# Performance work log

Hardware: AMD Instinct MI355X
Metric: run time of the kernel (lower is better)

The kernel has to match this reference:

```python
import jax, jax.numpy as jnp
import numpy as np

B, D, H, W = 1, 16, 16, 16
C, NH = 528, 8
HD = C // NH      # 66
K = 32            # retrieved memories per token


def setup_inputs() -> dict:
    key = jax.random.key(0)
    ks = jax.random.split(key, 4)
    x = jax.random.normal(ks[0], (B, D, H, W, C), jnp.float32)
    # simulated knn_memory.search output: (B, heads, N, K, 2[k/v], head_dim)
    knn_kv = jax.random.normal(ks[1], (B, NH, D * H * W, K, 2, HD), jnp.float32)
    w_qkv = jax.random.normal(ks[2], (3 * C, C), jnp.float32) * 0.02
    b_qkv = jnp.zeros((3 * C,), jnp.float32)
    w_proj = jax.random.normal(ks[3], (C, C), jnp.float32) * 0.02
    b_proj = jnp.zeros((C,), jnp.float32)
    return {"x": x, "knn_kv": knn_kv, "w_qkv": w_qkv, "b_qkv": b_qkv,
            "w_proj": w_proj, "b_proj": b_proj, "num_heads": NH}


def _l2norm(t):
    # F.normalize(t, dim=-1): t / max(||t||_2, eps)
    n = jnp.linalg.norm(t, axis=-1, keepdims=True)
    return t / jnp.maximum(n, 1e-12)


def _forward(x, knn_kv, w_qkv, b_qkv, w_proj, b_proj, num_heads):
    Bb, Dd, Hh, Ww, Cc = x.shape
    N = Dd * Hh * Ww
    hd = Cc // num_heads
    scaling = hd ** -0.5
    qkv = x.reshape(Bb * N, Cc) @ w_qkv.T + b_qkv
    qkv = qkv.reshape(Bb, N, 3, num_heads, hd).transpose(2, 0, 3, 1, 4)  # (3,B,h,N,hd)
    q, k, v = qkv[0], qkv[1], qkv[2]
    q = _l2norm(q)
    k = _l2norm(k)
    knn_k = knn_kv[..., 0, :]   # (B,h,N,K,hd)
    knn_v = knn_kv[..., 1, :]
    k_comb = jnp.concatenate([knn_k, k[..., None, :]], axis=-2)  # (B,h,N,K+1,hd)
    v_comb = jnp.concatenate([knn_v, v[..., None, :]], axis=-2)
    attn = jnp.einsum('bhnd,bhnkd->bhnk', q, k_comb) * scaling
    attn = jax.nn.softmax(attn, axis=-1)  # stable softmax
    out = jnp.einsum('bhnk,bhnkd->bhnd', attn, v_comb)  # (B,h,N,hd)
    out = out.transpose(0, 2, 1, 3).reshape(Bb * N, num_heads * hd)
    out = out @ w_proj.T + b_proj
    return out.reshape(Bb, Dd, Hh, Ww, Cc)


def reference(x, knn_kv, w_qkv, b_qkv, w_proj, b_proj, num_heads):
    return _forward(x, knn_kv, w_qkv, b_qkv, w_proj, b_proj, num_heads)
```

## Files before the change

### kernel.cpp

```cpp
#include <hip/hip_runtime.h>
#include <hip/hip_bf16.h>
#include <math.h>

#define N_POS 4096
#define C_DIM 528
#define NHEAD 8
#define HDIM  66
#define KNN   32
#define CQKV  1584
#define KP    544
#define NP1   1664
#define NP2   640

typedef __attribute__((ext_vector_type(8))) short short8;
typedef __attribute__((ext_vector_type(4))) float f32x4;
typedef __hip_bfloat16 bf16;

__global__ __launch_bounds__(256) void convpad3_kernel(
    const float* __restrict__ x, const float* __restrict__ wq,
    const float* __restrict__ wp,
    bf16* __restrict__ xb, bf16* __restrict__ wqb, bf16* __restrict__ wpb)
{
    int b = blockIdx.x;
    const float* src; bf16* dst; int Nr;
    if (b < N_POS)            { src = x;  dst = xb;  Nr = N_POS; }
    else if (b < N_POS + NP1) { b -= N_POS; src = wq; dst = wqb; Nr = CQKV; }
    else                      { b -= N_POS + NP1; src = wp; dst = wpb; Nr = C_DIM; }
    for (int c = threadIdx.x; c < KP; c += 256) {
        float v = (b < Nr && c < C_DIM) ? src[(size_t)b * C_DIM + c] : 0.0f;
        dst[(size_t)b * KP + c] = __float2bfloat16(v);
    }
}

template <bool BF16OUT>
__global__ __launch_bounds__(256) void gemm_mfma_kernel(
    const bf16* __restrict__ A, const bf16* __restrict__ B,
    const float* __restrict__ bias, void* __restrict__ Cv,
    int Nreal, int ldc, int nbx)
{
    __shared__ short8 As[512];
    __shared__ short8 Bs[512];

    const int tid  = threadIdx.x;
    const int lane = tid & 63;
    const int wid  = tid >> 6;

    const int nwg   = gridDim.x;
    const int chunk = nwg >> 3;
    const int swz   = (blockIdx.x & 7) * chunk + (blockIdx.x >> 3);
    const int bm = (swz / nbx) * 128;
    const int bn = (swz % nbx) * 128;

    const int r0 = tid >> 2;
    const int c0 = tid & 3;
    const bf16* Ag = A + (size_t)(bm + r0) * KP + c0 * 8;
    const bf16* Bg = B + (size_t)(bn + r0) * KP + c0 * 8;
    const size_t roff = (size_t)64 * KP;

    short8 a0 = *(const short8*)(Ag);
    short8 a1 = *(const short8*)(Ag + roff);
    short8 b0 = *(const short8*)(Bg);
    short8 b1 = *(const short8*)(Bg + roff);

    const int w0 = r0 * 4 + (c0 ^ (r0 & 3));
    const int w1 = w0 + 256;

    const int wm = (wid >> 1) * 64;
    const int wn = (wid & 1) * 64;
    const int arow = wm + (lane & 15);
    const int brow = wn + (lane & 15);
    const int apc  = lane >> 4;
    const int aslot = arow * 4 + (apc ^ (arow & 3));
    const int bslot = brow * 4 + (apc ^ (brow & 3));

    f32x4 acc[4][4];
    #pragma unroll
    for (int i = 0; i < 4; ++i)
        #pragma unroll
        for (int j = 0; j < 4; ++j)
            acc[i][j] = (f32x4){0.f, 0.f, 0.f, 0.f};

    for (int k0 = 0;; k0 += 32) {
        As[w0] = a0; As[w1] = a1;
        Bs[w0] = b0; Bs[w1] = b1;
        __syncthreads();
        if (k0 + 32 < KP) {
            const bf16* An = Ag + (k0 + 32);
            const bf16* Bn = Bg + (k0 + 32);
            a0 = *(const short8*)(An);
            a1 = *(const short8*)(An + roff);
            b0 = *(const short8*)(Bn);
            b1 = *(const short8*)(Bn + roff);
        }
        short8 af[4], bfr[4];
        #pragma unroll
        for (int f = 0; f < 4; ++f) af[f]  = As[aslot + f * 64];
        #pragma unroll
        for (int f = 0; f < 4; ++f) bfr[f] = Bs[bslot + f * 64];
        #pragma unroll
        for (int i = 0; i < 4; ++i)
            #pragma unroll
            for (int j = 0; j < 4; ++j)
                acc[i][j] = __builtin_amdgcn_mfma_f32_16x16x32_bf16(
                    af[i], bfr[j], acc[i][j], 0, 0, 0);
        if (k0 + 32 >= KP) break;
        __syncthreads();
    }

    #pragma unroll
    for (int i = 0; i < 4; ++i) {
        const int row = bm + wm + i * 16 + (lane >> 4) * 4;
        #pragma unroll
        for (int j = 0; j < 4; ++j) {
            const int col = bn + wn + j * 16 + (lane & 15);
            if (col < Nreal) {
                const float bv = bias[col];
                #pragma unroll
                for (int r = 0; r < 4; ++r) {
                    const float o = acc[i][j][r] + bv;
                    if (BF16OUT)
                        ((bf16*)Cv)[(size_t)(row + r) * ldc + col] = __float2bfloat16(o);
                    else
                        ((float*)Cv)[(size_t)(row + r) * ldc + col] = o;
                }
            }
        }
    }
}

__global__ __launch_bounds__(256) void attn_kernel(
    const bf16* __restrict__ qkv, const float* __restrict__ knn,
    bf16* __restrict__ out)
{
    const float scaling = 0.12309149097933272f;

    const int bid = blockIdx.x;
    const int tid = threadIdx.x;
    const int g0  = bid << 1;
    const int h   = g0 >> 12;
    const int n0  = g0 & 4095;
    const int n1  = n0 + 1;

    __shared__ float s_knn[2][KNN * 132];
    __shared__ float s_qkv[2][3 * HDIM];
    __shared__ float s_dot[2][KNN + 1];
    __shared__ float s_sc[2][2];

    const float4* kb0 = (const float4*)(knn + (size_t)g0 * (KNN * 132));
    const float4* kb1 = kb0 + KNN * 33;
    float4 r0[4], r1[4];
    float4 e0 = {0.f, 0.f, 0.f, 0.f}, e1 = {0.f, 0.f, 0.f, 0.f};
    #pragma unroll
    for (int i = 0; i < 4; ++i) r0[i] = kb0[tid + 256 * i];
    if (tid < 32) e0 = kb0[1024 + tid];
    #pragma unroll
    for (int i = 0; i < 4; ++i) r1[i] = kb1[tid + 256 * i];
    if (tid < 32) e1 = kb1[1024 + tid];

    const bf16* qp0 = qkv + (size_t)n0 * CQKV + h * HDIM;
    const bf16* qp1 = qp0 + CQKV;
    float qv0 = 0.f, qv1 = 0.f;
    int part = tid / HDIM, d66 = tid - part * HDIM;
    if (tid < 3 * HDIM) {
        qv0 = __bfloat162float(qp0[part * C_DIM + d66]);
        qv1 = __bfloat162float(qp1[part * C_DIM + d66]);
    }

    float4* s40 = (float4*)s_knn[0];
    float4* s41 = (float4*)s_knn[1];
    #pragma unroll
    for (int i = 0; i < 4; ++i) s40[tid + 256 * i] = r0[i];
    if (tid < 32) s40[1024 + tid] = e0;
    #pragma unroll
    for (int i = 0; i < 4; ++i) s41[tid + 256 * i] = r1[i];
    if (tid < 32) s41[1024 + tid] = e1;
    if (tid < 3 * HDIM) {
        s_qkv[0][tid] = qv0;
        s_qkv[1][tid] = qv1;
    }
    __syncthreads();

    const int team  = tid >> 7;
    const int ttid  = tid & 127;
    const int twave = ttid >> 6;
    const int lane  = tid & 63;
    const float* kK = s_knn[team];
    const float* Q  = &s_qkv[team][0];
    const float* KS = &s_qkv[team][HDIM];

    if (twave == 0) {
        const int j = lane >> 1, l2 = lane & 1;
        const float* kr = kK + j * 132;
        float p = 0.f;
        #pragma unroll
        for (int d = 0; d < HDIM / 2; ++d) p += Q[2 * d + l2] * kr[2 * d + l2];
        p += __shfl_xor(p, 1);
        if (l2 == 0) s_dot[team][j] = p;
    } else {
        float aq, ak, qk;
        {
            float qd = Q[lane], kd = KS[lane];
            aq = qd * qd; ak = kd * kd; qk = qd * kd;
            if (lane < 2) {
                float q2 = Q[64 + lane], k2 = KS[64 + lane];
                aq += q2 * q2; ak += k2 * k2; qk += q2 * k2;
            }
        }
        #pragma unroll
        for (int off = 32; off; off >>= 1) {
            aq += __shfl_xor(aq, off);
            ak += __shfl_xor(ak, off);
            qk += __shfl_xor(qk, off);
        }
        if (lane == 0) {
            const float iq = 1.0f / fmaxf(sqrtf(aq), 1e-12f);
            const float ik = 1.0f / fmaxf(sqrtf(ak), 1e-12f);
            s_sc[team][0] = iq * scaling;
            s_sc[team][1] = qk * iq * ik * scaling;
        }
    }
    __syncthreads();

    if (twave == 0) {
        float x = -3.4e38f;
        if (lane < 32)       x = s_dot[team][lane] * s_sc[team][0];
        else if (lane == 32) x = s_sc[team][1];
        float m = x;
        #pragma unroll
        for (int off = 32; off; off >>= 1) m = fmaxf(m, __shfl_xor(m, off));
        float e = (lane < 33) ? expf(x - m) : 0.f;
        float s = e;
        #pragma unroll
        for (int off = 32; off; off >>= 1) s += __shfl_xor(s, off);
        if (lane < 33) s_dot[team][lane] = e / s;
    }
    __syncthreads();

    if (ttid < HDIM) {
        const int d = ttid;
        float acc = s_dot[team][KNN] * s_qkv[team][2 * HDIM + d];
        #pragma unroll 8
        for (int j = 0; j < KNN; ++j)
            acc += s_dot[team][j] * kK[j * 132 + HDIM + d];
        const int n = team ? n1 : n0;
        out[(size_t)n * KP + h * HDIM + d] = __float2bfloat16(acc);
    }
    if (h == 0) {
        if (tid < 16)
            out[(size_t)n0 * KP + C_DIM + tid] = __float2bfloat16(0.f);
        else if (tid < 32)
            out[(size_t)n1 * KP + C_DIM + (tid - 16)] = __float2bfloat16(0.f);
    }
}

extern "C" void kernel_launch(void* const* d_in, const int* in_sizes, int n_in,
                              void* d_out, int out_size, void* d_ws, size_t ws_size,
                              hipStream_t stream)
{
    const float* x      = (const float*)d_in[0];
    const float* knn_kv = (const float*)d_in[1];
    const float* w_qkv  = (const float*)d_in[2];
    const float* b_qkv  = (const float*)d_in[3];
    const float* w_proj = (const float*)d_in[4];
    const float* b_proj = (const float*)d_in[5];
    float* out = (float*)d_out;

    char* ws = (char*)d_ws;
    bf16* qkvb = (bf16*)ws;
    bf16* xb   = (bf16*)(ws + 12976128);
    bf16* wqb  = (bf16*)(ws + 12976128 + 4456448);
    bf16* wpb  = (bf16*)(ws + 12976128 + 4456448 + 1810432);
    bf16* ab   = (bf16*)(ws + 12976128 + 4456448 + 1810432 + 696320);

    convpad3_kernel<<<N_POS + NP1 + NP2, 256, 0, stream>>>(x, w_qkv, w_proj, xb, wqb, wpb);

    gemm_mfma_kernel<true><<<dim3((NP1 / 128) * (N_POS / 128)), 256, 0, stream>>>(
        xb, wqb, b_qkv, qkvb, CQKV, CQKV, NP1 / 128);

    attn_kernel<<<dim3(NHEAD * N_POS / 2), 256, 0, stream>>>(qkvb, knn_kv, ab);

    gemm_mfma_kernel<false><<<dim3((NP2 / 128) * (N_POS / 128)), 256, 0, stream>>>(
        ab, wpb, b_proj, out, C_DIM, C_DIM, NP2 / 128);
}
```

Baseline: 171.8 us.

## Shrink GEMM tiles to 64x64 and double-buffer LDS via direct global-to-LDS loads

Both GEMMs now use 64x64 output tiles instead of 128x128, which quadruples the number of workgroups so the 256 CUs are better filled. Operand tiles are fetched with global_load_lds straight into a double-buffered, XOR-swizzled shared-memory layout, so the next K-slice streams in while MFMAs run on the current one. The cost is fewer MFMAs per LDS read and more redundant global traffic from the smaller tiles.

Result: no change. 171.8 us (-0.0%).

```diff
diff --git a/kernel.cpp b/kernel.cpp
--- a/kernel.cpp
+++ b/kernel.cpp
@@ -16,6 +16,9 @@
 typedef __attribute__((ext_vector_type(4))) float f32x4;
 typedef __hip_bfloat16 bf16;
 
+typedef const __attribute__((address_space(1))) void* gas1;
+typedef __attribute__((address_space(3))) void* las3;
+
 __global__ __launch_bounds__(256) void convpad3_kernel(
     const float* __restrict__ x, const float* __restrict__ wq,
     const float* __restrict__ wp,
@@ -38,8 +41,8 @@
     const float* __restrict__ bias, void* __restrict__ Cv,
     int Nreal, int ldc, int nbx)
 {
-    __shared__ short8 As[512];
-    __shared__ short8 Bs[512];
+    __shared__ bf16 As[2][64 * 32];
+    __shared__ bf16 Bs[2][64 * 32];
 
     const int tid  = threadIdx.x;
     const int lane = tid & 63;
@@ -48,80 +51,82 @@
     const int nwg   = gridDim.x;
     const int chunk = nwg >> 3;
     const int swz   = (blockIdx.x & 7) * chunk + (blockIdx.x >> 3);
-    const int bm = (swz / nbx) * 128;
-    const int bn = (swz % nbx) * 128;
-
-    const int r0 = tid >> 2;
-    const int c0 = tid & 3;
-    const bf16* Ag = A + (size_t)(bm + r0) * KP + c0 * 8;
-    const bf16* Bg = B + (size_t)(bn + r0) * KP + c0 * 8;
-    const size_t roff = (size_t)64 * KP;
-
-    short8 a0 = *(const short8*)(Ag);
-    short8 a1 = *(const short8*)(Ag + roff);
-    short8 b0 = *(const short8*)(Bg);
-    short8 b1 = *(const short8*)(Bg + roff);
-
-    const int w0 = r0 * 4 + (c0 ^ (r0 & 3));
-    const int w1 = w0 + 256;
-
-    const int wm = (wid >> 1) * 64;
-    const int wn = (wid & 1) * 64;
+    const int bm = (swz / nbx) * 64;
+    const int bn = (swz % nbx) * 64;
+
+    const int r   = (wid << 4) + (lane >> 2);
+    const int csw = ((lane & 3) ^ ((r >> 1) & 3)) << 3;
+
+    const bf16* Ag = A + (size_t)(bm + r) * KP + csw;
+    const bf16* Bg = B + (size_t)(bn + r) * KP + csw;
+
+    bf16* as0 = &As[0][0] + (wid << 4) * 32;
+    bf16* bs0 = &Bs[0][0] + (wid << 4) * 32;
+    const int BUF = 64 * 32;
+
+    const int wm = (wid >> 1) * 32;
+    const int wn = (wid & 1) * 32;
     const int arow = wm + (lane & 15);
     const int brow = wn + (lane & 15);
-    const int apc  = lane >> 4;
-    const int aslot = arow * 4 + (apc ^ (arow & 3));
-    const int bslot = brow * 4 + (apc ^ (brow & 3));
-
-    f32x4 acc[4][4];
-    #pragma unroll
-    for (int i = 0; i < 4; ++i)
-        #pragma unroll
-        for (int j = 0; j < 4; ++j)
+    const int seg  = lane >> 4;
+    const int aoff = (seg ^ ((arow >> 1) & 3)) << 3;
+    const int boff = (seg ^ ((brow >> 1) & 3)) << 3;
+
+    f32x4 acc[2][2];
+    #pragma unroll
+    for (int i = 0; i < 2; ++i)
+        #pragma unroll
+        for (int j = 0; j < 2; ++j)
             acc[i][j] = (f32x4){0.f, 0.f, 0.f, 0.f};
 
-    for (int k0 = 0;; k0 += 32) {
-        As[w0] = a0; As[w1] = a1;
-        Bs[w0] = b0; Bs[w1] = b1;
-        __syncthreads();
+    __builtin_amdgcn_global_load_lds((gas1)(Ag), (las3)(as0), 16, 0, 0);
+    __builtin_amdgcn_global_load_lds((gas1)(Bg), (las3)(bs0), 16, 0, 0);
+    __syncthreads();
+
+    int cur = 0;
+    for (int k0 = 0; k0 < KP; k0 += 32) {
         if (k0 + 32 < KP) {
-            const bf16* An = Ag + (k0 + 32);
-            const bf16* Bn = Bg + (k0 + 32);
-            a0 = *(const short8*)(An);
-            a1 = *(const short8*)(An + roff);
-            b0 = *(const short8*)(Bn);
-            b1 = *(const short8*)(Bn + roff);
-        }
-        short8 af[4], bfr[4];
-        #pragma unroll
-        for (int f = 0; f < 4; ++f) af[f]  = As[aslot + f * 64];
-        #pragma unroll
-        for (int f = 0; f < 4; ++f) bfr[f] = Bs[bslot + f * 64];
-        #pragma unroll
-        for (int i = 0; i < 4; ++i)
+            const int nb = cur ^ 1;
+            __builtin_amdgcn_global_load_lds((gas1)(Ag + k0 + 32), (las3)(as0 + nb * BUF), 16, 0, 0);
+            __builtin_amdgcn_global_load_lds((gas1)(Bg + k0 + 32), (las3)(bs0 + nb * BUF), 16, 0, 0);
+        }
+
+        const bf16* ab = &As[cur][0];
+        const bf16* bb = &Bs[cur][0];
+        short8 af[2], bfr[2];
+        #pragma unroll
+        for (int f = 0; f < 2; ++f)
+            af[f] = *(const short8*)&ab[(arow + f * 16) * 32 + aoff];
+        #pragma unroll
+        for (int f = 0; f < 2; ++f)
+            bfr[f] = *(const short8*)&bb[(brow + f * 16) * 32 + boff];
+
+        #pragma unroll
+        for (int i = 0; i < 2; ++i)
             #pragma unroll
-            for (int j = 0; j < 4; ++j)
+            for (int j = 0; j < 2; ++j)
                 acc[i][j] = __builtin_amdgcn_mfma_f32_16x16x32_bf16(
                     af[i], bfr[j], acc[i][j], 0, 0, 0);
-        if (k0 + 32 >= KP) break;
+
         __syncthreads();
-    }
-
-    #pragma unroll
-    for (int i = 0; i < 4; ++i) {
+        cur ^= 1;
+    }
+
+    #pragma unroll
+    for (int i = 0; i < 2; ++i) {
         const int row = bm + wm + i * 16 + (lane >> 4) * 4;
         #pragma unroll
-        for (int j = 0; j < 4; ++j) {
+        for (int j = 0; j < 2; ++j) {
             const int col = bn + wn + j * 16 + (lane & 15);
             if (col < Nreal) {
                 const float bv = bias[col];
                 #pragma unroll
-                for (int r = 0; r < 4; ++r) {
-                    const float o = acc[i][j][r] + bv;
+                for (int rr = 0; rr < 4; ++rr) {
+                    const float o = acc[i][j][rr] + bv;
                     if (BF16OUT)
-                        ((bf16*)Cv)[(size_t)(row + r) * ldc + col] = __float2bfloat16(o);
+                        ((bf16*)Cv)[(size_t)(row + rr) * ldc + col] = __float2bfloat16(o);
                     else
-                        ((float*)Cv)[(size_t)(row + r) * ldc + col] = o;
+                        ((float*)Cv)[(size_t)(row + rr) * ldc + col] = o;
                 }
             }
         }
@@ -274,11 +279,11 @@
 
     convpad3_kernel<<<N_POS + NP1 + NP2, 256, 0, stream>>>(x, w_qkv, w_proj, xb, wqb, wpb);
 
-    gemm_mfma_kernel<true><<<dim3((NP1 / 128) * (N_POS / 128)), 256, 0, stream>>>(
-        xb, wqb, b_qkv, qkvb, CQKV, CQKV, NP1 / 128);
+    gemm_mfma_kernel<true><<<dim3((NP1 / 64) * (N_POS / 64)), 256, 0, stream>>>(
+        xb, wqb, b_qkv, qkvb, CQKV, CQKV, NP1 / 64);
 
     attn_kernel<<<dim3(NHEAD * N_POS / 2), 256, 0, stream>>>(qkvb, knn_kv, ab);
 
-    gemm_mfma_kernel<false><<<dim3((NP2 / 128) * (N_POS / 128)), 256, 0, stream>>>(
-        ab, wpb, b_proj, out, C_DIM, C_DIM, NP2 / 128);
-}
+    gemm_mfma_kernel<false><<<dim3((NP2 / 64) * (N_POS / 64)), 256, 0, stream>>>(
+        ab, wpb, b_proj, out, C_DIM, C_DIM, NP2 / 64);
+}
```
